# Optimization experiments

Hardware: AMD Instinct MI355X
Metric: run time of the kernel (lower is better)

Reference implementation:

```python
import jax, jax.numpy as jnp
import numpy as np

WS = 8   # window size
NH = 6   # num heads
EPS = 1e-5


def _ln(x, g, b):
    # LayerNorm over last axis (biased variance, like torch)
    m = jnp.mean(x, axis=-1, keepdims=True)
    v = jnp.mean((x - m) ** 2, axis=-1, keepdims=True)
    return (x - m) / jnp.sqrt(v + EPS) * g + b


def _rel_pos_index(ws):
    coords = np.stack(np.meshgrid(np.arange(ws), np.arange(ws), indexing='ij'))  # (2,ws,ws)
    cf = coords.reshape(2, -1)                       # (2, ws*ws)
    rel = cf[:, :, None] - cf[:, None, :]            # (2, N, N)
    rel = rel.transpose(1, 2, 0).copy()              # (N, N, 2)
    rel[..., 0] += ws - 1
    rel[..., 1] += ws - 1
    rel[..., 0] *= 2 * ws - 1
    return jnp.asarray(rel.sum(-1))                  # (N, N) int


def setup_inputs() -> dict:
    key = jax.random.key(0)
    ks = jax.random.split(key, 8)
    B, C, H, W = 2, 192, 256, 256
    DF = 4 * C
    f = lambda k, shp, s: jax.random.normal(k, shp, jnp.float32) * s
    return {
        'x': f(ks[0], (B, C, H, W), 1.0),
        'ln1_g': jnp.ones((C,), jnp.float32), 'ln1_b': jnp.zeros((C,), jnp.float32),
        'qkv_w': f(ks[1], (C, 3 * C), 0.02), 'qkv_b': jnp.zeros((3 * C,), jnp.float32),
        'bias_table': f(ks[2], ((2 * WS - 1) ** 2, NH), 0.02),
        'proj_w': f(ks[3], (C, C), 0.02), 'proj_b': jnp.zeros((C,), jnp.float32),
        'ln2_g': jnp.ones((C,), jnp.float32), 'ln2_b': jnp.zeros((C,), jnp.float32),
        'fc1_w': f(ks[4], (DF, C), 0.02), 'fc1_b': jnp.zeros((DF,), jnp.float32),
        'fc2_w': f(ks[5], (DF, C), 0.02), 'fc2_b': jnp.zeros((DF,), jnp.float32),
        'fc3_w': f(ks[6], (C, DF), 0.02), 'fc3_b': jnp.zeros((C,), jnp.float32),
    }


def reference(x, ln1_g, ln1_b, qkv_w, qkv_b, bias_table, proj_w, proj_b,
              ln2_g, ln2_b, fc1_w, fc1_b, fc2_w, fc2_b, fc3_w, fc3_b):
    B, C, H, W = x.shape
    hd = C // NH
    scale = hd ** -0.5
    rp_idx = _rel_pos_index(WS)  # (N,N) static

    # norm1 over channels, back to (B,C,H,W) as in the source
    xn = _ln(x.transpose(0, 2, 3, 1), ln1_g, ln1_b).transpose(0, 3, 1, 2)

    # faithful replication: window_partition applied to (B,C,H,W) layout
    w = xn.reshape(B, C // WS, WS, H // WS, WS, W)
    w = w.transpose(0, 1, 3, 2, 4, 5).reshape(-1, WS * WS, C)  # (Bw, N, C)
    Bw, N, _ = w.shape

    # window attention (add_token=True, token_num=0 -> bias over full attn; mask=None)
    qkv = (w @ qkv_w + qkv_b).reshape(Bw, N, 3, NH, hd).transpose(2, 0, 3, 1, 4)
    q, k, v = qkv[0] * scale, qkv[1], qkv[2]       # (Bw, NH, N, hd)
    attn = jnp.einsum('bhnd,bhmd->bhnm', q, k)     # (Bw, NH, N, N)
    bias = bias_table[rp_idx].transpose(2, 0, 1)   # (NH, N, N)
    attn = jax.nn.softmax(attn + bias[None], axis=-1)
    o = jnp.einsum('bhnm,bhmd->bhnd', attn, v).transpose(0, 2, 1, 3).reshape(Bw, N, C)
    o = o @ proj_w + proj_b

    y = w + o  # residual on windowed (normalized) features, as in source

    # window_reverse back to (B, H, W, C)
    y = y.reshape(B, H // WS, W // WS, WS, WS, C)
    y = y.transpose(0, 1, 3, 2, 4, 5).reshape(B, H, W, C)

    z = _ln(y, ln2_g, ln2_b).transpose(0, 3, 1, 2)  # (B,C,H,W)

    # GatedFFN: sigmoid(fc1(z)) * fc2(z) -> fc3 (1x1 convs)
    h1 = jax.nn.sigmoid(jnp.einsum('bchw,oc->bohw', z, fc1_w) + fc1_b[None, :, None, None])
    h2 = jnp.einsum('bchw,oc->bohw', z, fc2_w) + fc2_b[None, :, None, None]
    out = jnp.einsum('bohw,po->bphw', h1 * h2, fc3_w) + fc3_b[None, :, None, None]
    return z + out
```

## Files before the change

### kernel.cpp

```cpp
#include <hip/hip_runtime.h>

typedef __attribute__((ext_vector_type(8))) short short8;
typedef __attribute__((ext_vector_type(4))) float f32x4;
typedef unsigned short u16;

#define MFMA(a,b,c) __builtin_amdgcn_mfma_f32_16x16x32_bf16((a),(b),(c),0,0,0)

static __device__ __forceinline__ float us2f(u16 u){
  union { unsigned x; float f; } v; v.x = ((unsigned)u) << 16; return v.f;
}
static __device__ __forceinline__ u16 f2us(float f){
  union { float f; unsigned x; } v; v.f = f;
  unsigned r = v.x + 0x7FFFu + ((v.x >> 16) & 1u);
  return (u16)(r >> 16);
}
template<int F32>
static __device__ __forceinline__ float ldin(const void* p, size_t i){
  if constexpr (F32) return ((const float*)p)[i];
  else               return us2f(((const u16*)p)[i]);
}

__global__ void k_detect(const unsigned* __restrict__ g1raw, int* __restrict__ flag)
{
  if (threadIdx.x == 0 && blockIdx.x == 0)
    flag[0] = (g1raw[0] == 0x3F800000u) ? 1 : 0;
}

template<int F32>
__global__ __launch_bounds__(256) void k_ln1_stats(const int* __restrict__ flag,
    const void* __restrict__ x, float* __restrict__ mean, float* __restrict__ rstd)
{
  if (flag[0] != F32) return;
  const unsigned bh = blockIdx.x;
  const unsigned w  = threadIdx.x;
  const unsigned b = bh >> 8, h = bh & 255u;
  const size_t base = (size_t)b*12582912u + (size_t)h*256u + w;
  float s = 0.f, q = 0.f;
  #pragma unroll 8
  for (int c = 0; c < 192; ++c) {
    float v = ldin<F32>(x, base + (size_t)c*65536u);
    s += v; q = fmaf(v, v, q);
  }
  float m = s * (1.f/192.f);
  float var = fmaf(-m, m, q * (1.f/192.f));
  unsigned p = bh*256u + w;
  mean[p] = m;
  rstd[p] = rsqrtf(fmaxf(var, 0.f) + 1e-5f);
}

template<int F32>
__global__ __launch_bounds__(256) void k_prep(const int* __restrict__ flag,
    const void* __restrict__ qkv_w, const void* __restrict__ proj_w,
    const void* __restrict__ fc1_w, const void* __restrict__ fc2_w,
    const void* __restrict__ fc3_w,
    u16* __restrict__ qkv_wT, u16* __restrict__ projT,
    u16* __restrict__ fc1c, u16* __restrict__ fc2c, u16* __restrict__ fc3c)
{
  if (flag[0] != F32) return;
  const unsigned i = blockIdx.x*256u + threadIdx.x;
  if (i < 110592u) {
    unsigned r = i / 192u, t = i - r*192u;
    qkv_wT[i] = f2us(ldin<F32>(qkv_w, (size_t)t*576u + r));
  } else if (i < 147456u) {
    unsigned j = i - 110592u, c = j / 192u, t = j - c*192u;
    projT[j] = f2us(ldin<F32>(proj_w, (size_t)t*192u + c));
  } else if (i < 294912u) {
    unsigned j = i - 147456u; fc1c[j] = f2us(ldin<F32>(fc1_w, j));
  } else if (i < 442368u) {
    unsigned j = i - 294912u; fc2c[j] = f2us(ldin<F32>(fc2_w, j));
  } else {
    unsigned j = i - 442368u; fc3c[j] = f2us(ldin<F32>(fc3_w, j));
  }
}

template<int F32>
__global__ __launch_bounds__(384) void k_attn(const int* __restrict__ flag,
    const void* __restrict__ x, const float* __restrict__ mean, const float* __restrict__ rstd,
    const void* __restrict__ g1, const void* __restrict__ b1,
    const u16* __restrict__ qkv_wT, const void* __restrict__ qkv_b,
    const void* __restrict__ bias_table,
    const u16* __restrict__ projT, const void* __restrict__ proj_b,
    const void* __restrict__ g2, const void* __restrict__ b2,
    u16* __restrict__ zbuf)
{
  if (flag[0] != F32) return;
  extern __shared__ char smem[];
  u16*  ws_w  = (u16*)(smem);
  u16*  ws_q  = (u16*)(smem + 24576);
  u16*  ws_k  = (u16*)(smem + 49152);
  u16*  ws_vT = (u16*)(smem + 73728);
  u16*  ws_P  = (u16*)(smem + 98304);
  float* ws_y = (float*)(smem + 98304);
  u16*  ws_o  = ws_q;

  const int tid  = threadIdx.x;
  const int wave = tid >> 6;
  const int lane = tid & 63;
  const int l16  = lane & 15;
  const int lhi  = lane >> 4;
  const unsigned bw = blockIdx.x;

  {
    const unsigned fbase = bw * 12288u;
    #pragma unroll 4
    for (int i = tid; i < 12288; i += 384) {
      unsigned f  = fbase + (unsigned)i;
      unsigned w_ = f & 255u;
      unsigned h2 = (f >> 8) & 7u;
      unsigned c2 = (f >> 11) & 7u;
      unsigned h1 = (f >> 14) & 31u;
      unsigned t19 = f >> 19;
      unsigned b_ = (t19 >= 24u) ? 1u : 0u;
      unsigned c1 = t19 - b_*24u;
      unsigned c  = c1*8u + c2;
      unsigned h  = h1*8u + h2;
      unsigned p  = (b_*256u + h)*256u + w_;
      size_t xi = ((size_t)(b_*192u + c)*256u + h)*256u + w_;
      float v = ldin<F32>(x, xi);
      v = (v - mean[p]) * rstd[p] * ldin<F32>(g1, c) + ldin<F32>(b1, c);
      ws_w[i] = f2us(v);
    }
  }
  __syncthreads();

  {
    f32x4 acc[4][6];
    #pragma unroll
    for (int mt = 0; mt < 4; ++mt)
      #pragma unroll
      for (int nt = 0; nt < 6; ++nt) acc[mt][nt] = (f32x4){0.f,0.f,0.f,0.f};
    const int jbase = wave * 96;
    #pragma unroll
    for (int kk = 0; kk < 6; ++kk) {
      const int kb = kk*32 + lhi*8;
      short8 a[4];
      #pragma unroll
      for (int mt = 0; mt < 4; ++mt)
        a[mt] = *(const short8*)(ws_w + (mt*16 + l16)*192 + kb);
      #pragma unroll
      for (int nt = 0; nt < 6; ++nt) {
        short8 bfr = *(const short8*)(qkv_wT + (size_t)(jbase + nt*16 + l16)*192 + kb);
        #pragma unroll
        for (int mt = 0; mt < 4; ++mt)
          acc[mt][nt] = MFMA(a[mt], bfr, acc[mt][nt]);
      }
    }
    #pragma unroll
    for (int nt = 0; nt < 6; ++nt) {
      const int j = jbase + nt*16 + l16;
      const int which = j / 192;
      const int rj = j - which*192;
      const int head = rj >> 5;
      const int d = rj & 31;
      const float qb = ldin<F32>(qkv_b, j);
      #pragma unroll
      for (int mt = 0; mt < 4; ++mt)
        #pragma unroll
        for (int jr = 0; jr < 4; ++jr) {
          const int n = mt*16 + lhi*4 + jr;
          float v = acc[mt][nt][jr] + qb;
          if (which == 0)      ws_q[head*2048 + n*32 + d] = f2us(v * 0.17677669529663687f);
          else if (which == 1) ws_k[head*2048 + n*32 + d] = f2us(v);
          else                 ws_vT[head*2048 + d*64 + n] = f2us(v);
        }
    }
  }
  __syncthreads();

  {
    const int head = wave;
    f32x4 sacc[4][4];
    #pragma unroll
    for (int tr = 0; tr < 4; ++tr)
      #pragma unroll
      for (int tc = 0; tc < 4; ++tc) sacc[tr][tc] = (f32x4){0.f,0.f,0.f,0.f};
    const int kb = lhi*8;
    short8 aq[4];
    #pragma unroll
    for (int tr = 0; tr < 4; ++tr)
      aq[tr] = *(const short8*)(ws_q + head*2048 + (tr*16 + l16)*32 + kb);
    #pragma unroll
    for (int tc = 0; tc < 4; ++tc) {
      short8 bk = *(const short8*)(ws_k + head*2048 + (tc*16 + l16)*32 + kb);
      #pragma unroll
      for (int tr = 0; tr < 4; ++tr)
        sacc[tr][tc] = MFMA(aq[tr], bk, sacc[tr][tc]);
    }
    #pragma unroll
    for (int tr = 0; tr < 4; ++tr)
      #pragma unroll
      for (int jr = 0; jr < 4; ++jr) {
        const int row = tr*16 + lhi*4 + jr;
        const int yi = row >> 3, xi = row & 7;
        float m = -1e30f;
        #pragma unroll
        for (int tc = 0; tc < 4; ++tc) {
          const int col = tc*16 + l16;
          const int yj = col >> 3, xj = col & 7;
          const int idx = (yi - yj + 7)*15 + (xi - xj + 7);
          float v = sacc[tr][tc][jr] + ldin<F32>(bias_table, idx*6 + head);
          sacc[tr][tc][jr] = v;
          m = fmaxf(m, v);
        }
        m = fmaxf(m, __shfl_xor(m, 1));
        m = fmaxf(m, __shfl_xor(m, 2));
        m = fmaxf(m, __shfl_xor(m, 4));
        m = fmaxf(m, __shfl_xor(m, 8));
        float ssum = 0.f;
        #pragma unroll
        for (int tc = 0; tc < 4; ++tc) {
          float e = __expf(sacc[tr][tc][jr] - m);
          sacc[tr][tc][jr] = e;
          ssum += e;
        }
        ssum += __shfl_xor(ssum, 1);
        ssum += __shfl_xor(ssum, 2);
        ssum += __shfl_xor(ssum, 4);
        ssum += __shfl_xor(ssum, 8);
        const float inv = 1.0f / ssum;
        #pragma unroll
        for (int tc = 0; tc < 4; ++tc) {
          const int col = tc*16 + l16;
          ws_P[head*4096 + row*64 + col] = f2us(sacc[tr][tc][jr] * inv);
        }
      }
  }
  __syncthreads();

  {
    const int head = wave;
    f32x4 oacc[4][2];
    #pragma unroll
    for (int tr = 0; tr < 4; ++tr)
      #pragma unroll
      for (int tdc = 0; tdc < 2; ++tdc) oacc[tr][tdc] = (f32x4){0.f,0.f,0.f,0.f};
    #pragma unroll
    for (int kk = 0; kk < 2; ++kk) {
      const int kb = kk*32 + lhi*8;
      short8 ap[4];
      #pragma unroll
      for (int tr = 0; tr < 4; ++tr)
        ap[tr] = *(const short8*)(ws_P + head*4096 + (tr*16 + l16)*64 + kb);
      #pragma unroll
      for (int tdc = 0; tdc < 2; ++tdc) {
        short8 bv = *(const short8*)(ws_vT + head*2048 + (tdc*16 + l16)*64 + kb);
        #pragma unroll
        for (int tr = 0; tr < 4; ++tr)
          oacc[tr][tdc] = MFMA(ap[tr], bv, oacc[tr][tdc]);
      }
    }
    #pragma unroll
    for (int tdc = 0; tdc < 2; ++tdc)
      #pragma unroll
      for (int tr = 0; tr < 4; ++tr)
        #pragma unroll
        for (int jr = 0; jr < 4; ++jr) {
          const int n = tr*16 + lhi*4 + jr;
          const int d = tdc*16 + l16;
          ws_o[n*192 + head*32 + d] = f2us(oacc[tr][tdc][jr]);
        }
  }
  __syncthreads();

  {
    const int cbase = wave * 32;
    f32x4 pacc[4][2];
    #pragma unroll
    for (int mt = 0; mt < 4; ++mt)
      #pragma unroll
      for (int nt = 0; nt < 2; ++nt) pacc[mt][nt] = (f32x4){0.f,0.f,0.f,0.f};
    #pragma unroll
    for (int kk = 0; kk < 6; ++kk) {
      const int kb = kk*32 + lhi*8;
      short8 a[4];
      #pragma unroll
      for (int mt = 0; mt < 4; ++mt)
        a[mt] = *(const short8*)(ws_o + (mt*16 + l16)*192 + kb);
      #pragma unroll
      for (int nt = 0; nt < 2; ++nt) {
        short8 bp = *(const short8*)(projT + (size_t)(cbase + nt*16 + l16)*192 + kb);
        #pragma unroll
        for (int mt = 0; mt < 4; ++mt)
          pacc[mt][nt] = MFMA(a[mt], bp, pacc[mt][nt]);
      }
    }
    #pragma unroll
    for (int nt = 0; nt < 2; ++nt) {
      const int cc = cbase + nt*16 + l16;
      const float pb = ldin<F32>(proj_b, cc);
      #pragma unroll
      for (int mt = 0; mt < 4; ++mt)
        #pragma unroll
        for (int jr = 0; jr < 4; ++jr) {
          const int n = mt*16 + lhi*4 + jr;
          ws_y[n*200 + cc] = pacc[mt][nt][jr] + pb + us2f(ws_w[n*192 + cc]);
        }
    }
  }
  __syncthreads();

  if (tid < 256) {
    const int pi = tid >> 2;
    const int part = tid & 3;
    const int c0 = part * 48;
    float vals[48];
    float s = 0.f, q = 0.f;
    #pragma unroll
    for (int c = 0; c < 48; ++c) {
      float v = ws_y[pi*200 + c0 + c];
      vals[c] = v; s += v; q = fmaf(v, v, q);
    }
    s += __shfl_xor(s, 1); s += __shfl_xor(s, 2);
    q += __shfl_xor(q, 1); q += __shfl_xor(q, 2);
    const float m = s * (1.f/192.f);
    const float var = fmaf(-m, m, q * (1.f/192.f));
    const float rs = rsqrtf(fmaxf(var, 0.f) + 1e-5f);
    const int b = (int)(bw >> 10);
    const int hh1 = (int)((bw >> 5) & 31u);
    const int ww1 = (int)(bw & 31u);
    const int h  = hh1*8 + (pi >> 3);
    const int w_ = ww1*8 + (pi & 7);
    size_t zo = ((size_t)((b*256 + h)*256 + w_))*192 + c0;
    #pragma unroll
    for (int c8 = 0; c8 < 6; ++c8) {
      short8 pk;
      #pragma unroll
      for (int j = 0; j < 8; ++j) {
        const int c = c8*8 + j;
        float z = (vals[c] - m)*rs*ldin<F32>(g2, c0+c) + ldin<F32>(b2, c0+c);
        pk[j] = (short)f2us(z);
      }
      *(short8*)(zbuf + zo + c8*8) = pk;
    }
  }
}

template<int F32>
__global__ __launch_bounds__(256) void k_ffn(const int* __restrict__ flag,
    const u16* __restrict__ zbuf,
    const u16* __restrict__ fc1c, const void* __restrict__ fc1_b,
    const u16* __restrict__ fc2c, const void* __restrict__ fc2_b,
    const u16* __restrict__ fc3c, const void* __restrict__ fc3_b,
    void* __restrict__ outv)
{
  if (flag[0] != F32) return;
  extern __shared__ char smem[];
  u16*  zt = (u16*)smem;
  u16*  ht = (u16*)(smem + 24576);
  float* ot = (float*)(smem + 24576);

  const int tid = threadIdx.x;
  const int wave = tid >> 6, lane = tid & 63;
  const int l16 = lane & 15, lhi = lane >> 4;
  const size_t p0 = (size_t)blockIdx.x * 64u;

  for (int i8 = tid; i8 < 1536; i8 += 256)
    *(short8*)(zt + i8*8) = *(const short8*)(zbuf + p0*192 + (size_t)i8*8);
  __syncthreads();

  {
    short8 a[4][6];
    #pragma unroll
    for (int mt = 0; mt < 4; ++mt)
      #pragma unroll
      for (int kk = 0; kk < 6; ++kk)
        a[mt][kk] = *(const short8*)(zt + (mt*16 + l16)*192 + kk*32 + lhi*8);
    for (int nt = 0; nt < 12; ++nt) {
      const int oc = wave*192 + nt*16 + l16;
      f32x4 acc1[4], acc2[4];
      #pragma unroll
      for (int mt = 0; mt < 4; ++mt) {
        acc1[mt] = (f32x4){0.f,0.f,0.f,0.f};
        acc2[mt] = (f32x4){0.f,0.f,0.f,0.f};
      }
      #pragma unroll
      for (int kk = 0; kk < 6; ++kk) {
        const int kb = kk*32 + lhi*8;
        short8 bf1 = *(const short8*)(fc1c + (size_t)oc*192 + kb);
        short8 bf2 = *(const short8*)(fc2c + (size_t)oc*192 + kb);
        #pragma unroll
        for (int mt = 0; mt < 4; ++mt) {
          acc1[mt] = MFMA(a[mt][kk], bf1, acc1[mt]);
          acc2[mt] = MFMA(a[mt][kk], bf2, acc2[mt]);
        }
      }
      const float bb1 = ldin<F32>(fc1_b, oc);
      const float bb2 = ldin<F32>(fc2_b, oc);
      #pragma unroll
      for (int mt = 0; mt < 4; ++mt)
        #pragma unroll
        for (int jr = 0; jr < 4; ++jr) {
          const int row = mt*16 + lhi*4 + jr;
          float h1 = acc1[mt][jr] + bb1;
          h1 = 1.f / (1.f + __expf(-h1));
          const float g = h1 * (acc2[mt][jr] + bb2);
          ht[row*768 + oc] = f2us(g);
        }
    }
  }
  __syncthreads();

  f32x4 facc[4][3];
  #pragma unroll
  for (int mt = 0; mt < 4; ++mt)
    #pragma unroll
    for (int nt = 0; nt < 3; ++nt) facc[mt][nt] = (f32x4){0.f,0.f,0.f,0.f};
  const int cbase = wave * 48;
  for (int kk = 0; kk < 24; ++kk) {
    const int kb = kk*32 + lhi*8;
    short8 a[4];
    #pragma unroll
    for (int mt = 0; mt < 4; ++mt)
      a[mt] = *(const short8*)(ht + (mt*16 + l16)*768 + kb);
    #pragma unroll
    for (int nt = 0; nt < 3; ++nt) {
      short8 bf = *(const short8*)(fc3c + (size_t)(cbase + nt*16 + l16)*768 + kb);
      #pragma unroll
      for (int mt = 0; mt < 4; ++mt)
        facc[mt][nt] = MFMA(a[mt], bf, facc[mt][nt]);
    }
  }
  __syncthreads();
  #pragma unroll
  for (int nt = 0; nt < 3; ++nt) {
    const int qc = cbase + nt*16 + l16;
    const float fb = ldin<F32>(fc3_b, qc);
    #pragma unroll
    for (int mt = 0; mt < 4; ++mt)
      #pragma unroll
      for (int jr = 0; jr < 4; ++jr) {
        const int row = mt*16 + lhi*4 + jr;
        const float v = facc[mt][nt][jr] + fb + us2f(zt[row*192 + qc]);
        ot[qc*65 + row] = v;
      }
  }
  __syncthreads();

  const int b  = (int)(p0 >> 16);
  const int h  = (int)((p0 >> 8) & 255u);
  const int w0 = (int)(p0 & 255u);
  for (int i = tid; i < 12288; i += 256) {
    const int qc = i >> 6, wi = i & 63;
    const size_t oi = ((size_t)(b*192 + qc)*256 + h)*256 + w0 + wi;
    const float v = ot[qc*65 + wi];
    if constexpr (F32) ((float*)outv)[oi] = v;
    else               ((u16*)outv)[oi] = f2us(v);
  }
}

extern "C" void kernel_launch(void* const* d_in, const int* in_sizes, int n_in,
                              void* d_out, int out_size, void* d_ws, size_t ws_size,
                              hipStream_t stream)
{
  const void* x       = d_in[0];
  const void* ln1_g   = d_in[1];
  const void* ln1_b   = d_in[2];
  const void* qkv_w   = d_in[3];
  const void* qkv_b   = d_in[4];
  const void* bias_tb = d_in[5];
  const void* proj_w  = d_in[6];
  const void* proj_b  = d_in[7];
  const void* ln2_g   = d_in[8];
  const void* ln2_b   = d_in[9];
  const void* fc1_w   = d_in[10];
  const void* fc1_b   = d_in[11];
  const void* fc2_w   = d_in[12];
  const void* fc2_b   = d_in[13];
  const void* fc3_w   = d_in[14];
  const void* fc3_b   = d_in[15];

  char* ws = (char*)d_ws;
  int*   flag   = (int*)(ws);
  float* meanp  = (float*)(ws + 256);
  float* rstdp  = (float*)(ws + 524544);
  u16*   qkv_wT = (u16*)(ws + 1048832);
  u16*   projT  = (u16*)(ws + 1270016);
  u16*   fc1c   = (u16*)(ws + 1343744);
  u16*   fc2c   = (u16*)(ws + 1638656);
  u16*   fc3c   = (u16*)(ws + 1933568);
  u16*   zbuf   = (u16*)(ws + 2228480);

  {
    void (*a0)(const int*, const void*, const float*, const float*, const void*, const void*,
               const u16*, const void*, const void*, const u16*, const void*, const void*,
               const void*, u16*) = k_attn<0>;
    void (*a1)(const int*, const void*, const float*, const float*, const void*, const void*,
               const u16*, const void*, const void*, const u16*, const void*, const void*,
               const void*, u16*) = k_attn<1>;
    void (*f0)(const int*, const u16*, const u16*, const void*, const u16*, const void*,
               const u16*, const void*, void*) = k_ffn<0>;
    void (*f1)(const int*, const u16*, const u16*, const void*, const u16*, const void*,
               const u16*, const void*, void*) = k_ffn<1>;
    hipFuncSetAttribute((const void*)a0, hipFuncAttributeMaxDynamicSharedMemorySize, 149504);
    hipFuncSetAttribute((const void*)a1, hipFuncAttributeMaxDynamicSharedMemorySize, 149504);
    hipFuncSetAttribute((const void*)f0, hipFuncAttributeMaxDynamicSharedMemorySize, 122880);
    hipFuncSetAttribute((const void*)f1, hipFuncAttributeMaxDynamicSharedMemorySize, 122880);
  }

  k_detect<<<1, 64, 0, stream>>>((const unsigned*)ln1_g, flag);

  k_ln1_stats<0><<<512, 256, 0, stream>>>(flag, x, meanp, rstdp);
  k_ln1_stats<1><<<512, 256, 0, stream>>>(flag, x, meanp, rstdp);

  k_prep<0><<<2304, 256, 0, stream>>>(flag, qkv_w, proj_w, fc1_w, fc2_w, fc3_w,
                                      qkv_wT, projT, fc1c, fc2c, fc3c);
  k_prep<1><<<2304, 256, 0, stream>>>(flag, qkv_w, proj_w, fc1_w, fc2_w, fc3_w,
                                      qkv_wT, projT, fc1c, fc2c, fc3c);

  k_attn<0><<<2048, 384, 149504, stream>>>(flag, x, meanp, rstdp, ln1_g, ln1_b,
                                           qkv_wT, qkv_b, bias_tb, projT, proj_b,
                                           ln2_g, ln2_b, zbuf);
  k_attn<1><<<2048, 384, 149504, stream>>>(flag, x, meanp, rstdp, ln1_g, ln1_b,
                                           qkv_wT, qkv_b, bias_tb, projT, proj_b,
                                           ln2_g, ln2_b, zbuf);

  k_ffn<0><<<2048, 256, 122880, stream>>>(flag, zbuf, fc1c, fc1_b, fc2c, fc2_b,
                                          fc3c, fc3_b, d_out);
  k_ffn<1><<<2048, 256, 122880, stream>>>(flag, zbuf, fc1c, fc1_b, fc2c, fc2_b,
                                          fc3c, fc3_b, d_out);
}
```

Before: 766.4 us.

## Drop dtype dispatch, double waves per block, swizzle LDS, restructure FFN chunking

Removes the runtime fp32/bf16 detection kernel and the duplicate template launches, so the code assumes fp32 inputs. The attention kernel now runs 768 threads with finer per-wave tiles, and its LDS tiles use XOR swizzling to avoid bank conflicts. The FFN is restructured to 512 threads: the hidden dimension is processed in three 256-wide chunks that accumulate into fc3, and outputs are written straight from registers. LDS use drops, which allows higher occupancy, at the cost of extra syncs and smaller per-wave tiles.

```diff
diff --git a/kernel.cpp b/kernel.cpp
--- a/kernel.cpp
+++ b/kernel.cpp
@@ -14,31 +14,28 @@
   unsigned r = v.x + 0x7FFFu + ((v.x >> 16) & 1u);
   return (u16)(r >> 16);
 }
-template<int F32>
-static __device__ __forceinline__ float ldin(const void* p, size_t i){
-  if constexpr (F32) return ((const float*)p)[i];
-  else               return us2f(((const u16*)p)[i]);
-}
-
-__global__ void k_detect(const unsigned* __restrict__ g1raw, int* __restrict__ flag)
+static __device__ __forceinline__ int swzN(int row, int col, int C){
+  int ch = col >> 3;
+  ch = (ch & ~7) | ((ch ^ row) & 7);
+  return row*C + ch*8 + (col & 7);
+}
+static __device__ __forceinline__ int swz32(int row, int col){
+  int ch = col >> 3;
+  ch = (ch ^ row ^ (row >> 2)) & 3;
+  return row*32 + ch*8 + (col & 7);
+}
+
+__global__ __launch_bounds__(256) void k_ln1_stats(const float* __restrict__ x,
+    float* __restrict__ mean, float* __restrict__ rstd)
 {
-  if (threadIdx.x == 0 && blockIdx.x == 0)
-    flag[0] = (g1raw[0] == 0x3F800000u) ? 1 : 0;
-}
-
-template<int F32>
-__global__ __launch_bounds__(256) void k_ln1_stats(const int* __restrict__ flag,
-    const void* __restrict__ x, float* __restrict__ mean, float* __restrict__ rstd)
-{
-  if (flag[0] != F32) return;
   const unsigned bh = blockIdx.x;
   const unsigned w  = threadIdx.x;
   const unsigned b = bh >> 8, h = bh & 255u;
-  const size_t base = (size_t)b*12582912u + (size_t)h*256u + w;
+  const float* px = x + (size_t)b*12582912u + (size_t)h*256u + w;
   float s = 0.f, q = 0.f;
-  #pragma unroll 8
+  #pragma unroll 16
   for (int c = 0; c < 192; ++c) {
-    float v = ldin<F32>(x, base + (size_t)c*65536u);
+    float v = px[(size_t)c*65536u];
     s += v; q = fmaf(v, v, q);
   }
   float m = s * (1.f/192.f);
@@ -48,42 +45,39 @@
   rstd[p] = rsqrtf(fmaxf(var, 0.f) + 1e-5f);
 }
 
-template<int F32>
-__global__ __launch_bounds__(256) void k_prep(const int* __restrict__ flag,
-    const void* __restrict__ qkv_w, const void* __restrict__ proj_w,
-    const void* __restrict__ fc1_w, const void* __restrict__ fc2_w,
-    const void* __restrict__ fc3_w,
+__global__ __launch_bounds__(256) void k_prep(
+    const float* __restrict__ qkv_w, const float* __restrict__ proj_w,
+    const float* __restrict__ fc1_w, const float* __restrict__ fc2_w,
+    const float* __restrict__ fc3_w,
     u16* __restrict__ qkv_wT, u16* __restrict__ projT,
     u16* __restrict__ fc1c, u16* __restrict__ fc2c, u16* __restrict__ fc3c)
 {
-  if (flag[0] != F32) return;
   const unsigned i = blockIdx.x*256u + threadIdx.x;
   if (i < 110592u) {
     unsigned r = i / 192u, t = i - r*192u;
-    qkv_wT[i] = f2us(ldin<F32>(qkv_w, (size_t)t*576u + r));
+    qkv_wT[i] = f2us(qkv_w[(size_t)t*576u + r]);
   } else if (i < 147456u) {
     unsigned j = i - 110592u, c = j / 192u, t = j - c*192u;
-    projT[j] = f2us(ldin<F32>(proj_w, (size_t)t*192u + c));
+    projT[j] = f2us(proj_w[(size_t)t*192u + c]);
   } else if (i < 294912u) {
-    unsigned j = i - 147456u; fc1c[j] = f2us(ldin<F32>(fc1_w, j));
+    unsigned j = i - 147456u; fc1c[j] = f2us(fc1_w[j]);
   } else if (i < 442368u) {
-    unsigned j = i - 294912u; fc2c[j] = f2us(ldin<F32>(fc2_w, j));
+    unsigned j = i - 294912u; fc2c[j] = f2us(fc2_w[j]);
   } else {
-    unsigned j = i - 442368u; fc3c[j] = f2us(ldin<F32>(fc3_w, j));
-  }
-}
-
-template<int F32>
-__global__ __launch_bounds__(384) void k_attn(const int* __restrict__ flag,
-    const void* __restrict__ x, const float* __restrict__ mean, const float* __restrict__ rstd,
-    const void* __restrict__ g1, const void* __restrict__ b1,
-    const u16* __restrict__ qkv_wT, const void* __restrict__ qkv_b,
-    const void* __restrict__ bias_table,
-    const u16* __restrict__ projT, const void* __restrict__ proj_b,
-    const void* __restrict__ g2, const void* __restrict__ b2,
+    unsigned j = i - 442368u; fc3c[j] = f2us(fc3_w[j]);
+  }
+}
+
+__global__ __launch_bounds__(768, 3) void k_attn(
+    const float* __restrict__ x, const float* __restrict__ mean,
+    const float* __restrict__ rstd,
+    const float* __restrict__ g1, const float* __restrict__ b1,
+    const u16* __restrict__ qkv_wT, const float* __restrict__ qkv_b,
+    const float* __restrict__ bias_table,
+    const u16* __restrict__ projT, const float* __restrict__ proj_b,
+    const float* __restrict__ g2, const float* __restrict__ b2,
     u16* __restrict__ zbuf)
 {
-  if (flag[0] != F32) return;
   extern __shared__ char smem[];
   u16*  ws_w  = (u16*)(smem);
   u16*  ws_q  = (u16*)(smem + 24576);
@@ -103,7 +97,7 @@
   {
     const unsigned fbase = bw * 12288u;
     #pragma unroll 4
-    for (int i = tid; i < 12288; i += 384) {
+    for (int i = tid; i < 12288; i += 768) {
       unsigned f  = fbase + (unsigned)i;
       unsigned w_ = f & 255u;
       unsigned h2 = (f >> 8) & 7u;
@@ -116,81 +110,82 @@
       unsigned h  = h1*8u + h2;
       unsigned p  = (b_*256u + h)*256u + w_;
       size_t xi = ((size_t)(b_*192u + c)*256u + h)*256u + w_;
-      float v = ldin<F32>(x, xi);
-      v = (v - mean[p]) * rstd[p] * ldin<F32>(g1, c) + ldin<F32>(b1, c);
-      ws_w[i] = f2us(v);
+      float v = x[xi];
+      v = (v - mean[p]) * rstd[p] * g1[c] + b1[c];
+      int row = i / 192, col = i - row*192;
+      ws_w[swzN(row, col, 192)] = f2us(v);
     }
   }
   __syncthreads();
 
   {
-    f32x4 acc[4][6];
+    f32x4 acc[4][3];
     #pragma unroll
     for (int mt = 0; mt < 4; ++mt)
       #pragma unroll
-      for (int nt = 0; nt < 6; ++nt) acc[mt][nt] = (f32x4){0.f,0.f,0.f,0.f};
-    const int jbase = wave * 96;
+      for (int nt = 0; nt < 3; ++nt) acc[mt][nt] = (f32x4){0.f,0.f,0.f,0.f};
+    const int jb = wave * 48;
+    const int which = wave >> 2;
     #pragma unroll
     for (int kk = 0; kk < 6; ++kk) {
       const int kb = kk*32 + lhi*8;
       short8 a[4];
       #pragma unroll
       for (int mt = 0; mt < 4; ++mt)
-        a[mt] = *(const short8*)(ws_w + (mt*16 + l16)*192 + kb);
-      #pragma unroll
-      for (int nt = 0; nt < 6; ++nt) {
-        short8 bfr = *(const short8*)(qkv_wT + (size_t)(jbase + nt*16 + l16)*192 + kb);
+        a[mt] = *(const short8*)(ws_w + swzN(mt*16 + l16, kb, 192));
+      #pragma unroll
+      for (int nt = 0; nt < 3; ++nt) {
+        short8 bfr = *(const short8*)(qkv_wT + (size_t)(jb + nt*16 + l16)*192 + kb);
         #pragma unroll
         for (int mt = 0; mt < 4; ++mt)
           acc[mt][nt] = MFMA(a[mt], bfr, acc[mt][nt]);
       }
     }
     #pragma unroll
-    for (int nt = 0; nt < 6; ++nt) {
-      const int j = jbase + nt*16 + l16;
-      const int which = j / 192;
+    for (int nt = 0; nt < 3; ++nt) {
+      const int j = jb + nt*16 + l16;
       const int rj = j - which*192;
       const int head = rj >> 5;
       const int d = rj & 31;
-      const float qb = ldin<F32>(qkv_b, j);
+      const float qb = qkv_b[j];
       #pragma unroll
       for (int mt = 0; mt < 4; ++mt)
         #pragma unroll
         for (int jr = 0; jr < 4; ++jr) {
           const int n = mt*16 + lhi*4 + jr;
           float v = acc[mt][nt][jr] + qb;
-          if (which == 0)      ws_q[head*2048 + n*32 + d] = f2us(v * 0.17677669529663687f);
-          else if (which == 1) ws_k[head*2048 + n*32 + d] = f2us(v);
-          else                 ws_vT[head*2048 + d*64 + n] = f2us(v);
+          if (which == 0)      ws_q[head*2048 + swz32(n, d)] = f2us(v * 0.17677669529663687f);
+          else if (which == 1) ws_k[head*2048 + swz32(n, d)] = f2us(v);
+          else                 ws_vT[head*2048 + swzN(d, n, 64)] = f2us(v);
         }
     }
   }
   __syncthreads();
 
   {
-    const int head = wave;
-    f32x4 sacc[4][4];
-    #pragma unroll
-    for (int tr = 0; tr < 4; ++tr)
-      #pragma unroll
-      for (int tc = 0; tc < 4; ++tc) sacc[tr][tc] = (f32x4){0.f,0.f,0.f,0.f};
-    const int kb = lhi*8;
-    short8 aq[4];
-    #pragma unroll
-    for (int tr = 0; tr < 4; ++tr)
-      aq[tr] = *(const short8*)(ws_q + head*2048 + (tr*16 + l16)*32 + kb);
+    const int head = wave >> 1, half = wave & 1;
+    f32x4 sacc[2][4];
+    #pragma unroll
+    for (int ti = 0; ti < 2; ++ti)
+      #pragma unroll
+      for (int tc = 0; tc < 4; ++tc) sacc[ti][tc] = (f32x4){0.f,0.f,0.f,0.f};
+    const int kb0 = lhi*8;
+    short8 aq[2];
+    #pragma unroll
+    for (int ti = 0; ti < 2; ++ti)
+      aq[ti] = *(const short8*)(ws_q + head*2048 + swz32((half*2 + ti)*16 + l16, kb0));
     #pragma unroll
     for (int tc = 0; tc < 4; ++tc) {
-      short8 bk = *(const short8*)(ws_k + head*2048 + (tc*16 + l16)*32 + kb);
-      #pragma unroll
-      for (int tr = 0; tr < 4; ++tr)
-        sacc[tr][tc] = MFMA(aq[tr], bk, sacc[tr][tc]);
-    }
-    #pragma unroll
-    for (int tr = 0; tr < 4; ++tr)
+      short8 bk = *(const short8*)(ws_k + head*2048 + swz32(tc*16 + l16, kb0));
+      #pragma unroll
+      for (int ti = 0; ti < 2; ++ti)
+        sacc[ti][tc] = MFMA(aq[ti], bk, sacc[ti][tc]);
+    }
+    #pragma unroll
+    for (int ti = 0; ti < 2; ++ti)
       #pragma unroll
       for (int jr = 0; jr < 4; ++jr) {
-        const int row = tr*16 + lhi*4 + jr;
+        const int row = (half*2 + ti)*16 + lhi*4 + jr;
         const int yi = row >> 3, xi = row & 7;
         float m = -1e30f;
         #pragma unroll
@@ -198,8 +193,8 @@
           const int col = tc*16 + l16;
           const int yj = col >> 3, xj = col & 7;
           const int idx = (yi - yj + 7)*15 + (xi - xj + 7);
-          float v = sacc[tr][tc][jr] + ldin<F32>(bias_table, idx*6 + head);
-          sacc[tr][tc][jr] = v;
+          float v = sacc[ti][tc][jr] + bias_table[idx*6 + head];
+          sacc[ti][tc][jr] = v;
           m = fmaxf(m, v);
         }
         m = fmaxf(m, __shfl_xor(m, 1));
@@ -209,8 +204,8 @@
         float ssum = 0.f;
         #pragma unroll
         for (int tc = 0; tc < 4; ++tc) {
-          float e = __expf(sacc[tr][tc][jr] - m);
-          sacc[tr][tc][jr] = e;
+          float e = __expf(sacc[ti][tc][jr] - m);
+          sacc[ti][tc][jr] = e;
           ssum += e;
         }
         ssum += __shfl_xor(ssum, 1);
@@ -221,81 +216,71 @@
         #pragma unroll
         for (int tc = 0; tc < 4; ++tc) {
           const int col = tc*16 + l16;
-          ws_P[head*4096 + row*64 + col] = f2us(sacc[tr][tc][jr] * inv);
+          ws_P[head*4096 + swzN(row, col, 64)] = f2us(sacc[ti][tc][jr] * inv);
         }
       }
   }
   __syncthreads();
 
   {
-    const int head = wave;
-    f32x4 oacc[4][2];
-    #pragma unroll
-    for (int tr = 0; tr < 4; ++tr)
-      #pragma unroll
-      for (int tdc = 0; tdc < 2; ++tdc) oacc[tr][tdc] = (f32x4){0.f,0.f,0.f,0.f};
+    const int head = wave >> 1, half = wave & 1;
+    f32x4 oacc[2][2];
+    #pragma unroll
+    for (int ti = 0; ti < 2; ++ti)
+      #pragma unroll
+      for (int td = 0; td < 2; ++td) oacc[ti][td] = (f32x4){0.f,0.f,0.f,0.f};
     #pragma unroll
     for (int kk = 0; kk < 2; ++kk) {
       const int kb = kk*32 + lhi*8;
-      short8 ap[4];
-      #pragma unroll
-      for (int tr = 0; tr < 4; ++tr)
-        ap[tr] = *(const short8*)(ws_P + head*4096 + (tr*16 + l16)*64 + kb);
-      #pragma unroll
-      for (int tdc = 0; tdc < 2; ++tdc) {
-        short8 bv = *(const short8*)(ws_vT + head*2048 + (tdc*16 + l16)*64 + kb);
-        #pragma unroll
-        for (int tr = 0; tr < 4; ++tr)
-          oacc[tr][tdc] = MFMA(ap[tr], bv, oacc[tr][tdc]);
-      }
-    }
-    #pragma unroll
-    for (int tdc = 0; tdc < 2; ++tdc)
-      #pragma unroll
-      for (int tr = 0; tr < 4; ++tr)
+      short8 ap[2];
+      #pragma unroll
+      for (int ti = 0; ti < 2; ++ti)
+        ap[ti] = *(const short8*)(ws_P + head*4096 + swzN((half*2 + ti)*16 + l16, kb, 64));
+      #pragma unroll
+      for (int td = 0; td < 2; ++td) {
+        short8 bv = *(const short8*)(ws_vT + head*2048 + swzN(td*16 + l16, kb, 64));
+        #pragma unroll
+        for (int ti = 0; ti < 2; ++ti)
+          oacc[ti][td] = MFMA(ap[ti], bv, oacc[ti][td]);
+      }
+    }
+    #pragma unroll
+    for (int td = 0; td < 2; ++td)
+      #pragma unroll
+      for (int ti = 0; ti < 2; ++ti)
         #pragma unroll
         for (int jr = 0; jr < 4; ++jr) {
-          const int n = tr*16 + lhi*4 + jr;
-          const int d = tdc*16 + l16;
-          ws_o[n*192 + head*32 + d] = f2us(oacc[tr][tdc][jr]);
+          const int n = (half*2 + ti)*16 + lhi*4 + jr;
+          const int d = td*16 + l16;
+          ws_o[swzN(n, head*32 + d, 192)] = f2us(oacc[ti][td][jr]);
         }
   }
   __syncthreads();
 
   {
-    const int cbase = wave * 32;
-    f32x4 pacc[4][2];
-    #pragma unroll
-    for (int mt = 0; mt < 4; ++mt)
-      #pragma unroll
-      for (int nt = 0; nt < 2; ++nt) pacc[mt][nt] = (f32x4){0.f,0.f,0.f,0.f};
+    const int cb = wave * 16;
+    f32x4 pacc[4];
+    #pragma unroll
+    for (int mt = 0; mt < 4; ++mt) pacc[mt] = (f32x4){0.f,0.f,0.f,0.f};
     #pragma unroll
     for (int kk = 0; kk < 6; ++kk) {
       const int kb = kk*32 + lhi*8;
-      short8 a[4];
-      #pragma unroll
-      for (int mt = 0; mt < 4; ++mt)
-        a[mt] = *(const short8*)(ws_o + (mt*16 + l16)*192 + kb);
-      #pragma unroll
-      for (int nt = 0; nt < 2; ++nt) {
-        short8 bp = *(const short8*)(projT + (size_t)(cbase + nt*16 + l16)*192 + kb);
-        #pragma unroll
-        for (int mt = 0; mt < 4; ++mt)
-          pacc[mt][nt] = MFMA(a[mt], bp, pacc[mt][nt]);
-      }
-    }
-    #pragma unroll
-    for (int nt = 0; nt < 2; ++nt) {
-      const int cc = cbase + nt*16 + l16;
-      const float pb = ldin<F32>(proj_b, cc);
-      #pragma unroll
-      for (int mt = 0; mt < 4; ++mt)
-        #pragma unroll
-        for (int jr = 0; jr < 4; ++jr) {
-          const int n = mt*16 + lhi*4 + jr;
-          ws_y[n*200 + cc] = pacc[mt][nt][jr] + pb + us2f(ws_w[n*192 + cc]);
-        }
-    }
+      short8 bp = *(const short8*)(projT + (size_t)(cb + l16)*192 + kb);
+      #pragma unroll
+      for (int mt = 0; mt < 4; ++mt) {
+        short8 a = *(const short8*)(ws_o + swzN(mt*16 + l16, kb, 192));
+        pacc[mt] = MFMA(a, bp, pacc[mt]);
+      }
+    }
+    const int cc = cb + l16;
+    const float pb = proj_b[cc];
+    #pragma unroll
+    for (int mt = 0; mt < 4; ++mt)
+      #pragma unroll
+      for (int jr = 0; jr < 4; ++jr) {
+        const int n = mt*16 + lhi*4 + jr;
+        ws_y[n*193 + cc] = pacc[mt][jr] + pb + us2f(ws_w[swzN(n, cc, 192)]);
+      }
   }
   __syncthreads();
 
@@ -307,7 +292,7 @@
     float s = 0.f, q = 0.f;
     #pragma unroll
     for (int c = 0; c < 48; ++c) {
-      float v = ws_y[pi*200 + c0 + c];
+      float v = ws_y[pi*193 + c0 + c];
       vals[c] = v; s += v; q = fmaf(v, v, q);
     }
     s += __shfl_xor(s, 1); s += __shfl_xor(s, 2);
@@ -327,7 +312,7 @@
       #pragma unroll
       for (int j = 0; j < 8; ++j) {
         const int c = c8*8 + j;
-        float z = (vals[c] - m)*rs*ldin<F32>(g2, c0+c) + ldin<F32>(b2, c0+c);
+        float z = (vals[c] - m)*rs*g2[c0+c] + b2[c0+c];
         pk[j] = (short)f2us(z);
       }
       *(short8*)(zbuf + zo + c8*8) = pk;
@@ -335,187 +320,167 @@
   }
 }
 
-template<int F32>
-__global__ __launch_bounds__(256) void k_ffn(const int* __restrict__ flag,
+__global__ __launch_bounds__(512, 4) void k_ffn(
     const u16* __restrict__ zbuf,
-    const u16* __restrict__ fc1c, const void* __restrict__ fc1_b,
-    const u16* __restrict__ fc2c, const void* __restrict__ fc2_b,
-    const u16* __restrict__ fc3c, const void* __restrict__ fc3_b,
-    void* __restrict__ outv)
+    const u16* __restrict__ fc1c, const float* __restrict__ fc1_b,
+    const u16* __restrict__ fc2c, const float* __restrict__ fc2_b,
+    const u16* __restrict__ fc3c, const float* __restrict__ fc3_b,
+    float* __restrict__ out)
 {
-  if (flag[0] != F32) return;
   extern __shared__ char smem[];
-  u16*  zt = (u16*)smem;
-  u16*  ht = (u16*)(smem + 24576);
-  float* ot = (float*)(smem + 24576);
+  u16* zt  = (u16*)smem;
+  u16* htc = (u16*)(smem + 24576);
 
   const int tid = threadIdx.x;
   const int wave = tid >> 6, lane = tid & 63;
   const int l16 = lane & 15, lhi = lane >> 4;
   const size_t p0 = (size_t)blockIdx.x * 64u;
 
-  for (int i8 = tid; i8 < 1536; i8 += 256)
-    *(short8*)(zt + i8*8) = *(const short8*)(zbuf + p0*192 + (size_t)i8*8);
-  __syncthreads();
-
-  {
-    short8 a[4][6];
-    #pragma unroll
-    for (int mt = 0; mt < 4; ++mt)
-      #pragma unroll
-      for (int kk = 0; kk < 6; ++kk)
-        a[mt][kk] = *(const short8*)(zt + (mt*16 + l16)*192 + kk*32 + lhi*8);
-    for (int nt = 0; nt < 12; ++nt) {
-      const int oc = wave*192 + nt*16 + l16;
-      f32x4 acc1[4], acc2[4];
-      #pragma unroll
-      for (int mt = 0; mt < 4; ++mt) {
-        acc1[mt] = (f32x4){0.f,0.f,0.f,0.f};
-        acc2[mt] = (f32x4){0.f,0.f,0.f,0.f};
-      }
+  for (int i8 = tid; i8 < 1536; i8 += 512) {
+    int row = i8 / 24, ch = i8 - row*24;
+    int chs = (ch & 24) | ((ch ^ row) & 7);
+    *(short8*)(zt + row*192 + chs*8) =
+        *(const short8*)(zbuf + (p0 + row)*192 + ch*8);
+  }
+  __syncthreads();
+
+  f32x4 facc[3][2];
+  #pragma unroll
+  for (int tm = 0; tm < 3; ++tm)
+    #pragma unroll
+    for (int tn = 0; tn < 2; ++tn) facc[tm][tn] = (f32x4){0.f,0.f,0.f,0.f};
+  const int wm = wave >> 1, wn = wave & 1;
+  const int cb = wm*48, pbx = wn*32;
+  const int jb = wave*32;
+
+  #pragma unroll
+  for (int rep = 0; rep < 3; ++rep) {
+    {
+      f32x4 acc1[4][2], acc2[4][2];
+      #pragma unroll
+      for (int mt = 0; mt < 4; ++mt)
+        #pragma unroll
+        for (int nt = 0; nt < 2; ++nt) {
+          acc1[mt][nt] = (f32x4){0.f,0.f,0.f,0.f};
+          acc2[mt][nt] = (f32x4){0.f,0.f,0.f,0.f};
+        }
       #pragma unroll
       for (int kk = 0; kk < 6; ++kk) {
         const int kb = kk*32 + lhi*8;
-        short8 bf1 = *(const short8*)(fc1c + (size_t)oc*192 + kb);
-        short8 bf2 = *(const short8*)(fc2c + (size_t)oc*192 + kb);
-        #pragma unroll
-        for (int mt = 0; mt < 4; ++mt) {
-          acc1[mt] = MFMA(a[mt][kk], bf1, acc1[mt]);
-          acc2[mt] = MFMA(a[mt][kk], bf2, acc2[mt]);
-        }
-      }
-      const float bb1 = ldin<F32>(fc1_b, oc);
-      const float bb2 = ldin<F32>(fc2_b, oc);
-      #pragma unroll
-      for (int mt = 0; mt < 4; ++mt)
-        #pragma unroll
-        for (int jr = 0; jr < 4; ++jr) {
-          const int row = mt*16 + lhi*4 + jr;
-          float h1 = acc1[mt][jr] + bb1;
-          h1 = 1.f / (1.f + __expf(-h1));
-          const float g = h1 * (acc2[mt][jr] + bb2);
-          ht[row*768 + oc] = f2us(g);
-        }
-    }
-  }
-  __syncthreads();
-
-  f32x4 facc[4][3];
-  #pragma unroll
-  for (int mt = 0; mt < 4; ++mt)
-    #pragma unroll
-    for (int nt = 0; nt < 3; ++nt) facc[mt][nt] = (f32x4){0.f,0.f,0.f,0.f};
-  const int cbase = wave * 48;
-  for (int kk = 0; kk < 24; ++kk) {
-    const int kb = kk*32 + lhi*8;
-    short8 a[4];
-    #pragma unroll
-    for (int mt = 0; mt < 4; ++mt)
-      a[mt] = *(const short8*)(ht + (mt*16 + l16)*768 + kb);
-    #pragma unroll
-    for (int nt = 0; nt < 3; ++nt) {
-      short8 bf = *(const short8*)(fc3c + (size_t)(cbase + nt*16 + l16)*768 + kb);
-      #pragma unroll
-      for (int mt = 0; mt < 4; ++mt)
-        facc[mt][nt] = MFMA(a[mt], bf, facc[mt][nt]);
-    }
-  }
-  __syncthreads();
-  #pragma unroll
-  for (int nt = 0; nt < 3; ++nt) {
-    const int qc = cbase + nt*16 + l16;
-    const float fb = ldin<F32>(fc3_b, qc);
-    #pragma unroll
-    for (int mt = 0; mt < 4; ++mt)
-      #pragma unroll
-      for (int jr = 0; jr < 4; ++jr) {
-        const int row = mt*16 + lhi*4 + jr;
-        const float v = facc[mt][nt][jr] + fb + us2f(zt[row*192 + qc]);
-        ot[qc*65 + row] = v;
-      }
-  }
-  __syncthreads();
+        short8 a[4];
+        #pragma unroll
+        for (int mt = 0; mt < 4; ++mt)
+          a[mt] = *(const short8*)(zt + swzN(mt*16 + l16, kb, 192));
+        #pragma unroll
+        for (int nt = 0; nt < 2; ++nt) {
+          const int oc = rep*256 + jb + nt*16 + l16;
+          short8 bf1 = *(const short8*)(fc1c + (size_t)oc*192 + kb);
+          short8 bf2 = *(const short8*)(fc2c + (size_t)oc*192 + kb);
+          #pragma unroll
+          for (int mt = 0; mt < 4; ++mt) {
+            acc1[mt][nt] = MFMA(a[mt], bf1, acc1[mt][nt]);
+            acc2[mt][nt] = MFMA(a[mt], bf2, acc2[mt][nt]);
+          }
+        }
+      }
+      #pragma unroll
+      for (int nt = 0; nt < 2; ++nt) {
+        const int ocl = jb + nt*16 + l16;
+        const int oc  = rep*256 + ocl;
+        const float bb1 = fc1_b[oc];
+        const float bb2 = fc2_b[oc];
+        #pragma unroll
+        for (int mt = 0; mt < 4; ++mt)
+          #pragma unroll
+          for (int jr = 0; jr < 4; ++jr) {
+            const int row = mt*16 + lhi*4 + jr;
+            float h1 = acc1[mt][nt][jr] + bb1;
+            h1 = 1.f / (1.f + __expf(-h1));
+            const float g = h1 * (acc2[mt][nt][jr] + bb2);
+            htc[swzN(row, ocl, 256)] = f2us(g);
+          }
+      }
+    }
+    __syncthreads();
+
+    #pragma unroll
+    for (int kk = 0; kk < 8; ++kk) {
+      const int kb = kk*32 + lhi*8;
+      short8 bfr[2];
+      #pragma unroll
+      for (int tn = 0; tn < 2; ++tn)
+        bfr[tn] = *(const short8*)(htc + swzN(pbx + tn*16 + l16, kb, 256));
+      #pragma unroll
+      for (int tm = 0; tm < 3; ++tm) {
+        short8 aw = *(const short8*)(fc3c + (size_t)(cb + tm*16 + l16)*768
+                                     + rep*256 + kb);
+        #pragma unroll
+        for (int tn = 0; tn < 2; ++tn)
+          facc[tm][tn] = MFMA(aw, bfr[tn], facc[tm][tn]);
+      }
+    }
+    __syncthreads();
+  }
 
   const int b  = (int)(p0 >> 16);
   const int h  = (int)((p0 >> 8) & 255u);
   const int w0 = (int)(p0 & 255u);
-  for (int i = tid; i < 12288; i += 256) {
-    const int qc = i >> 6, wi = i & 63;
-    const size_t oi = ((size_t)(b*192 + qc)*256 + h)*256 + w0 + wi;
-    const float v = ot[qc*65 + wi];
-    if constexpr (F32) ((float*)outv)[oi] = v;
-    else               ((u16*)outv)[oi] = f2us(v);
-  }
+  #pragma unroll
+  for (int tm = 0; tm < 3; ++tm)
+    #pragma unroll
+    for (int jr = 0; jr < 4; ++jr) {
+      const int qc = cb + tm*16 + lhi*4 + jr;
+      const float fb = fc3_b[qc];
+      #pragma unroll
+      for (int tn = 0; tn < 2; ++tn) {
+        const int pix = pbx + tn*16 + l16;
+        const float v = facc[tm][tn][jr] + fb + us2f(zt[swzN(pix, qc, 192)]);
+        out[((size_t)(b*192 + qc)*256 + h)*256 + w0 + pix] = v;
+      }
+    }
 }
 
 extern "C" void kernel_launch(void* const* d_in, const int* in_sizes, int n_in,
                               void* d_out, int out_size, void* d_ws, size_t ws_size,
                               hipStream_t stream)
 {
-  const void* x       = d_in[0];
-  const void* ln1_g   = d_in[1];
-  const void* ln1_b   = d_in[2];
-  const void* qkv_w   = d_in[3];
-  const void* qkv_b   = d_in[4];
-  const void* bias_tb = d_in[5];
-  const void* proj_w  = d_in[6];
-  const void* proj_b  = d_in[7];
-  const void* ln2_g   = d_in[8];
-  const void* ln2_b   = d_in[9];
-  const void* fc1_w   = d_in[10];
-  const void* fc1_b   = d_in[11];
-  const void* fc2_w   = d_in[12];
-  const void* fc2_b   = d_in[13];
-  const void* fc3_w   = d_in[14];
-  const void* fc3_b   = d_in[15];
+  const float* x       = (const float*)d_in[0];
+  const float* ln1_g   = (const float*)d_in[1];
+  const float* ln1_b   = (const float*)d_in[2];
+  const float* qkv_w   = (const float*)d_in[3];
+  const float* qkv_b   = (const float*)d_in[4];
+  const float* bias_tb = (const float*)d_in[5];
+  const float* proj_w  = (const float*)d_in[6];
+  const float* proj_b  = (const float*)d_in[7];
+  const float* ln2_g   = (const float*)d_in[8];
+  const float* ln2_b   = (const float*)d_in[9];
+  const float* fc1_w   = (const float*)d_in[10];
+  const float* fc1_b   = (const float*)d_in[11];
+  const float* fc2_w   = (const float*)d_in[12];
+  const float* fc2_b   = (const float*)d_in[13];
+  const float* fc3_w   = (const float*)d_in[14];
+  const float* fc3_b   = (const float*)d_in[15];
+  float* outp = (float*)d_out;
 
   char* ws = (char*)d_ws;
-  int*   flag   = (int*)(ws);
-  float* meanp  = (float*)(ws + 256);
-  float* rstdp  = (float*)(ws + 524544);
-  u16*   qkv_wT = (u16*)(ws + 1048832);
-  u16*   projT  = (u16*)(ws + 1270016);
-  u16*   fc1c   = (u16*)(ws + 1343744);
-  u16*   fc2c   = (u16*)(ws + 1638656);
-  u16*   fc3c   = (u16*)(ws + 1933568);
-  u16*   zbuf   = (u16*)(ws + 2228480);
-
-  {
-    void (*a0)(const int*, const void*, const float*, const float*, const void*, const void*,
-               const u16*, const void*, const void*, const u16*, const void*, const void*,
-               const void*, u16*) = k_attn<0>;
-    void (*a1)(const int*, const void*, const float*, const float*, const void*, const void*,
-               const u16*, const void*, const void*, const u16*, const void*, const void*,
-               const void*, u16*) = k_attn<1>;
-    void (*f0)(const int*, const u16*, const u16*, const void*, const u16*, const void*,
-               const u16*, const void*, void*) = k_ffn<0>;
-    void (*f1)(const int*, const u16*, const u16*, const void*, const u16*, const void*,
-               const u16*, const void*, void*) = k_ffn<1>;
-    hipFuncSetAttribute((const void*)a0, hipFuncAttributeMaxDynamicSharedMemorySize, 149504);
-    hipFuncSetAttribute((const void*)a1, hipFuncAttributeMaxDynamicSharedMemorySize, 149504);
-    hipFuncSetAttribute((const void*)f0, hipFuncAttributeMaxDynamicSharedMemorySize, 122880);
-    hipFuncSetAttribute((const void*)f1, hipFuncAttributeMaxDynamicSharedMemorySize, 122880);
-  }
-
-  k_detect<<<1, 64, 0, stream>>>((const unsigned*)ln1_g, flag);
-
-  k_ln1_stats<0><<<512, 256, 0, stream>>>(flag, x, meanp, rstdp);
-  k_ln1_stats<1><<<512, 256, 0, stream>>>(flag, x, meanp, rstdp);
-
-  k_prep<0><<<2304, 256, 0, stream>>>(flag, qkv_w, proj_w, fc1_w, fc2_w, fc3_w,
-                                      qkv_wT, projT, fc1c, fc2c, fc3c);
-  k_prep<1><<<2304, 256, 0, stream>>>(flag, qkv_w, proj_w, fc1_w, fc2_w, fc3_w,
-                                      qkv_wT, projT, fc1c, fc2c, fc3c);
-
-  k_attn<0><<<2048, 384, 149504, stream>>>(flag, x, meanp, rstdp, ln1_g, ln1_b,
-                                           qkv_wT, qkv_b, bias_tb, projT, proj_b,
-                                           ln2_g, ln2_b, zbuf);
-  k_attn<1><<<2048, 384, 149504, stream>>>(flag, x, meanp, rstdp, ln1_g, ln1_b,
-                                           qkv_wT, qkv_b, bias_tb, projT, proj_b,
-                                           ln2_g, ln2_b, zbuf);
-
-  k_ffn<0><<<2048, 256, 122880, stream>>>(flag, zbuf, fc1c, fc1_b, fc2c, fc2_b,
-                                          fc3c, fc3_b, d_out);
-  k_ffn<1><<<2048, 256, 122880, stream>>>(flag, zbuf, fc1c, fc1_b, fc2c, fc2_b,
-                                          fc3c, fc3_b, d_out);
-}
+  float* meanp  = (float*)(ws);
+  float* rstdp  = (float*)(ws + 524288);
+  u16*   qkv_wT = (u16*)(ws + 1048576);
+  u16*   projT  = (u16*)(ws + 1269760);
+  u16*   fc1c   = (u16*)(ws + 1343488);
+  u16*   fc2c   = (u16*)(ws + 1638400);
+  u16*   fc3c   = (u16*)(ws + 1933312);
+  u16*   zbuf   = (u16*)(ws + 2228224);
+
+  hipFuncSetAttribute((const void*)k_attn, hipFuncAttributeMaxDynamicSharedMemorySize, 147712);
+  hipFuncSetAttribute((const void*)k_ffn,  hipFuncAttributeMaxDynamicSharedMemorySize, 57344);
+
+  k_ln1_stats<<<512, 256, 0, stream>>>(x, meanp, rstdp);
+  k_prep<<<2304, 256, 0, stream>>>(qkv_w, proj_w, fc1_w, fc2_w, fc3_w,
+                                   qkv_wT, projT, fc1c, fc2c, fc3c);
+  k_attn<<<2048, 768, 147712, stream>>>(x, meanp, rstdp, ln1_g, ln1_b,
+                                        qkv_wT, qkv_b, bias_tb, projT, proj_b,
+                                        ln2_g, ln2_b, zbuf);
+  k_ffn<<<2048, 512, 57344, stream>>>(zbuf, fc1c, fc1_b, fc2c, fc2_b,
+                                      fc3c, fc3_b, outp);
+}
```

Result: slower. 811.1 us (+5.8%).
